# Kernel tuning notes

Hardware: AMD Instinct MI355X
Metric: run time of the kernel (lower is better)

Reference implementation:

```python
import jax, jax.numpy as jnp
import numpy as np

EMB = 1024
HEADS = 16


def setup_inputs() -> dict:
    key = jax.random.key(0)
    ks = jax.random.split(key, 9)
    s = 1.0 / np.sqrt(EMB)
    x = jax.random.normal(ks[0], (2, 2048, EMB), dtype=jnp.float32)
    Wq = jax.random.normal(ks[1], (EMB, EMB), dtype=jnp.float32) * s
    bq = jnp.zeros((EMB,), dtype=jnp.float32)
    Wk = jax.random.normal(ks[2], (EMB, EMB), dtype=jnp.float32) * s
    bk = jnp.zeros((EMB,), dtype=jnp.float32)
    Wv = jax.random.normal(ks[3], (EMB, EMB), dtype=jnp.float32) * s
    bv = jnp.zeros((EMB,), dtype=jnp.float32)
    Wo = jax.random.normal(ks[4], (EMB, EMB), dtype=jnp.float32) * s
    bo = jnp.zeros((EMB,), dtype=jnp.float32)
    return {"x": x, "Wq": Wq, "bq": bq, "Wk": Wk, "bk": bk,
            "Wv": Wv, "bv": bv, "Wo": Wo, "bo": bo}


def reference(x, Wq, bq, Wk, bk, Wv, bv, Wo, bo):
    b, n, e = x.shape
    h = HEADS
    d = e // h
    # q/k/v projections -> [b, h, n, d]
    def split_heads(t):
        return t.reshape(b, n, h, d).transpose(0, 2, 1, 3)
    q = split_heads(x @ Wq.T + bq)
    k = split_heads(x @ Wk.T + bk)
    v = split_heads(x @ Wv.T + bv)
    # NOTE: original scales by sqrt(emb_size), not sqrt(head_dim)
    scaling = jnp.sqrt(jnp.float32(e))
    energy = jnp.einsum('bhqd,bhkd->bhqk', q, k)  # [b,h,n,n]
    att = jax.nn.softmax(energy / scaling, axis=-1)
    out = jnp.einsum('bhqk,bhkd->bhqd', att, v)
    out = out.transpose(0, 2, 1, 3).reshape(b, n, e)
    return out @ Wo.T + bo
```

## Files before the change

### kernel.cpp

```cpp
#include <hip/hip_runtime.h>


typedef short short8  __attribute__((ext_vector_type(8)));
typedef float floatx4 __attribute__((ext_vector_type(4)));

#define SEQ   2048
#define BATCH 2
#define NH    16
#define HD    64
#define EMB   1024

#define QSCALE 0.045084220027780106f

__device__ __forceinline__ unsigned short f32_bf16(float f) {
    unsigned int u = __float_as_uint(f);
    u += 0x7FFF + ((u >> 16) & 1);
    return (unsigned short)(u >> 16);
}

__device__ __forceinline__ unsigned int pk_bf16(float lo, float hi) {
    return __builtin_amdgcn_perm(__float_as_uint(hi) + 0x8000u,
                                 __float_as_uint(lo) + 0x8000u, 0x07060302u);
}

__device__ __forceinline__ void gl_lds16(const unsigned short* g,
                                         unsigned short* l) {
    __builtin_amdgcn_global_load_lds(
        (const __attribute__((address_space(1))) unsigned int*)g,
        (__attribute__((address_space(3))) unsigned int*)l, 16, 0, 0);
}

__global__ __launch_bounds__(256) void convert_all(
        const float* __restrict__ x,  const float* __restrict__ wq,
        const float* __restrict__ wk, const float* __restrict__ wv,
        const float* __restrict__ wo, unsigned short* __restrict__ dst) {
    int i = (blockIdx.x * 256 + threadIdx.x) * 4;
    const float* src; int off;
    if      (i < 4194304) { src = x;  off = 0; }
    else if (i < 5242880) { src = wq; off = 4194304; }
    else if (i < 6291456) { src = wk; off = 5242880; }
    else if (i < 7340032) { src = wv; off = 6291456; }
    else                  { src = wo; off = 7340032; }
    float4 v = *(const float4*)(src + (i - off));
    uint2 o;
    o.x = pk_bf16(v.x, v.y);
    o.y = pk_bf16(v.z, v.w);
    *(uint2*)(dst + i) = o;
}

template <int MODE>
__device__ __forceinline__ void gemm_bt_core(
        unsigned short (* __restrict__ sA)[64],
        unsigned short (* __restrict__ sB)[64],
        const unsigned short* __restrict__ A,
        const unsigned short* __restrict__ B,
        const float* __restrict__ bias,
        unsigned short* __restrict__ outb) {
    const int t    = threadIdx.x;
    const int wave = t >> 6, lane = t & 63;
    const int l15  = lane & 15, quad = lane >> 4;
    const int wm   = (wave >> 1) * 64, wn = (wave & 1) * 64;
    const int m0   = blockIdx.y * 128,  n0 = blockIdx.x * 128;
    const int srow = lane >> 3;
    const int sch  = ((lane & 7) ^ srow) * 8;

    floatx4 acc[4][4] = {};

    for (int k0 = 0; k0 < EMB; k0 += 64) {
        for (int i = 0; i < 4; ++i) {
            int rr  = wave * 32 + i * 8;
            int row = rr + srow;
            gl_lds16(&A[(size_t)(m0 + row) * EMB + k0 + sch], &sA[0][0] + rr * 64);
            gl_lds16(&B[(size_t)(n0 + row) * EMB + k0 + sch], &sB[0][0] + rr * 64);
        }
        __syncthreads();
        for (int ks = 0; ks < 2; ++ks) {
            const int ch = (((ks * 4) + quad) ^ (l15 & 7)) * 8;
            short8 af[4], bf[4];
            for (int i = 0; i < 4; ++i)
                af[i] = *(const short8*)&sA[wm + i * 16 + l15][ch];
            for (int j = 0; j < 4; ++j)
                bf[j] = *(const short8*)&sB[wn + j * 16 + l15][ch];
            for (int i = 0; i < 4; ++i)
                for (int j = 0; j < 4; ++j)
                    acc[i][j] = __builtin_amdgcn_mfma_f32_16x16x32_bf16(
                        af[i], bf[j], acc[i][j], 0, 0, 0);
        }
        __syncthreads();
    }
    if (MODE == 2) {
        for (int i = 0; i < 4; ++i) {
            int row = m0 + wm + i * 16 + quad * 4;
            int bb  = row >> 11, seq = row & 2047;
            for (int j = 0; j < 4; ++j) {
                int col = n0 + wn + j * 16 + l15;
                float bv = bias[col];
                int vtrow = (bb * 16 + (col >> 6)) * 64 + (col & 63);
                uint2 pk;
                pk.x = pk_bf16(acc[i][j][0] + bv, acc[i][j][1] + bv);
                pk.y = pk_bf16(acc[i][j][2] + bv, acc[i][j][3] + bv);
                *(uint2*)&outb[(size_t)vtrow * SEQ + seq] = pk;
            }
        }
    } else {
        const float sc2 = (MODE == 1) ? QSCALE : 1.0f;
        for (int i = 0; i < 4; ++i) {
            int row = m0 + wm + i * 16 + quad * 4;
            for (int j = 0; j < 4; ++j) {
                int col = n0 + wn + j * 16 + l15;
                float bv = bias[col];
                for (int r = 0; r < 4; ++r) {
                    float v = (acc[i][j][r] + bv) * sc2;
                    outb[(size_t)(row + r) * EMB + col] = f32_bf16(v);
                }
            }
        }
    }
}

__global__ __launch_bounds__(256, 3) void gemm_qkv(
        const unsigned short* __restrict__ xb,
        const unsigned short* __restrict__ wq,
        const unsigned short* __restrict__ wk,
        const unsigned short* __restrict__ wv,
        const float* __restrict__ bq, const float* __restrict__ bk,
        const float* __restrict__ bv,
        unsigned short* __restrict__ Q, unsigned short* __restrict__ K,
        unsigned short* __restrict__ VT) {
    __shared__ unsigned short sA[128][64];
    __shared__ unsigned short sB[128][64];
    if      (blockIdx.z == 0) gemm_bt_core<1>(sA, sB, xb, wq, bq, Q);
    else if (blockIdx.z == 1) gemm_bt_core<0>(sA, sB, xb, wk, bk, K);
    else                      gemm_bt_core<2>(sA, sB, xb, wv, bv, VT);
}

__global__ __launch_bounds__(256) void gemm_out(
        const unsigned short* __restrict__ A,
        const unsigned short* __restrict__ B,
        const float* __restrict__ bias, float* __restrict__ out) {
    __shared__ unsigned short sA[128][64];
    __shared__ unsigned short sB[64][64];
    const int t    = threadIdx.x;
    const int wave = t >> 6, lane = t & 63;
    const int l15  = lane & 15, quad = lane >> 4;
    const int wm   = wave * 32;
    const int m0   = blockIdx.y * 128,  n0 = blockIdx.x * 64;
    const int srow = lane >> 3;
    const int sch  = ((lane & 7) ^ srow) * 8;

    floatx4 acc[2][4] = {};

    for (int k0 = 0; k0 < EMB; k0 += 64) {
        {
            for (int i = 0; i < 4; ++i) {
                int rr = wave * 32 + i * 8;
                gl_lds16(&A[(size_t)(m0 + rr + srow) * EMB + k0 + sch],
                         &sA[0][0] + rr * 64);
            }
            for (int i = 0; i < 2; ++i) {
                int rr = wave * 16 + i * 8;
                gl_lds16(&B[(size_t)(n0 + rr + srow) * EMB + k0 + sch],
                         &sB[0][0] + rr * 64);
            }
        }
        __syncthreads();
        for (int ks = 0; ks < 2; ++ks) {
            const int ch = (((ks * 4) + quad) ^ (l15 & 7)) * 8;
            short8 af[2], bf[4];
            for (int i = 0; i < 2; ++i)
                af[i] = *(const short8*)&sA[wm + i * 16 + l15][ch];
            for (int j = 0; j < 4; ++j)
                bf[j] = *(const short8*)&sB[j * 16 + l15][ch];
            for (int i = 0; i < 2; ++i)
                for (int j = 0; j < 4; ++j)
                    acc[i][j] = __builtin_amdgcn_mfma_f32_16x16x32_bf16(
                        af[i], bf[j], acc[i][j], 0, 0, 0);
        }
        __syncthreads();
    }
    for (int i = 0; i < 2; ++i) {
        int row = m0 + wm + i * 16 + quad * 4;
        for (int j = 0; j < 4; ++j) {
            int col = n0 + j * 16 + l15;
            float bv = bias[col];
            for (int r = 0; r < 4; ++r)
                out[(size_t)(row + r) * EMB + col] = acc[i][j][r] + bv;
        }
    }
}

__global__ __launch_bounds__(512) void attn(
        const unsigned short* __restrict__ Q,
        const unsigned short* __restrict__ K,
        const unsigned short* __restrict__ VT,
        unsigned short* __restrict__ O) {
    __shared__ unsigned short sK [3][64][64];
    __shared__ unsigned short sVT[3][64][64];
    __shared__ unsigned short sP [128][72];
    const int t    = threadIdx.x;
    const int wave = t >> 6, lane = t & 63;
    const int l15  = lane & 15, quad = lane >> 4;
    const int bh   = blockIdx.x;
    const int b    = bh >> 4, h = bh & 15;
    const int q0   = blockIdx.y * 128;
    const size_t rowbase = (size_t)b * SEQ;
    const int colbase  = h * HD;
    const size_t vtbase = (size_t)bh * HD * SEQ;
    const int srow = lane >> 3;
    const int sch  = ((lane & 7) ^ srow) * 8;

    short8 qf[2];
    for (int ks = 0; ks < 2; ++ks)
        qf[ks] = *(const short8*)&Q[(rowbase + q0 + wave * 16 + l15) * EMB
                                    + colbase + ks * 32 + quad * 8];

    float l_part = 0.f;
    floatx4 o_acc[4] = {};

    const int rr  = wave * 8;
    const int row = rr + srow;

    gl_lds16(&K[(rowbase + row) * EMB + colbase + sch], &sK[0][0][0] + rr * 64);
    gl_lds16(&VT[vtbase + (size_t)row * SEQ + sch],     &sVT[0][0][0] + rr * 64);

    int cur = 0;
    for (int it = 0; it < SEQ / 64; ++it) {
        if (it < SEQ / 64 - 1) {
            int nb = cur + 1; if (nb == 3) nb = 0;
            int kt = (it + 1) * 64;
            gl_lds16(&K[(rowbase + kt + row) * EMB + colbase + sch],
                     &sK[nb][0][0] + rr * 64);
            gl_lds16(&VT[vtbase + (size_t)row * SEQ + kt + sch],
                     &sVT[nb][0][0] + rr * 64);
            asm volatile("s_waitcnt vmcnt(2)" ::: "memory");
        } else {
            asm volatile("s_waitcnt vmcnt(0)" ::: "memory");
        }
        asm volatile("s_barrier" ::: "memory");

        const unsigned short (*cK)[64]  = sK[cur];
        const unsigned short (*cVT)[64] = sVT[cur];

        floatx4 s[4] = {};
        for (int ks = 0; ks < 2; ++ks) {
            const int ch = (((ks * 4) + quad) ^ (l15 & 7)) * 8;
            short8 kf[4];
            for (int mi = 0; mi < 4; ++mi)
                kf[mi] = *(const short8*)&cK[mi * 16 + l15][ch];
            for (int mi = 0; mi < 4; ++mi)
                s[mi] = __builtin_amdgcn_mfma_f32_16x16x32_bf16(
                    kf[mi], qf[ks], s[mi], 0, 0, 0);
        }

        {
            int prow = wave * 16 + l15;
            float lp = l_part;
            for (int mi = 0; mi < 4; ++mi) {
                float p0 = __builtin_amdgcn_exp2f(s[mi][0]);
                float p1 = __builtin_amdgcn_exp2f(s[mi][1]);
                float p2 = __builtin_amdgcn_exp2f(s[mi][2]);
                float p3 = __builtin_amdgcn_exp2f(s[mi][3]);
                lp += (p0 + p1) + (p2 + p3);
                uint2 pk;
                pk.x = pk_bf16(p0, p1);
                pk.y = pk_bf16(p2, p3);
                *(uint2*)&sP[prow][mi * 16 + quad * 4] = pk;
            }
            l_part = lp;
        }

        for (int ks = 0; ks < 2; ++ks) {
            const int ch = (((ks * 4) + quad) ^ (l15 & 7)) * 8;
            short8 vf[4];
            for (int mi = 0; mi < 4; ++mi)
                vf[mi] = *(const short8*)&cVT[mi * 16 + l15][ch];
            short8 pf = *(const short8*)&sP[wave * 16 + l15][ks * 32 + quad * 8];
            for (int mi = 0; mi < 4; ++mi)
                o_acc[mi] = __builtin_amdgcn_mfma_f32_16x16x32_bf16(
                    vf[mi], pf, o_acc[mi], 0, 0, 0);
        }
        cur = cur + 1; if (cur == 3) cur = 0;
    }

    float la = l_part;
    la += __shfl_xor(la, 16, 64);
    la += __shfl_xor(la, 32, 64);
    const float inv_l = 1.0f / la;

    {
        int prow = wave * 16 + l15;
        for (int mi = 0; mi < 4; ++mi) {
            uint2 pk;
            pk.x = pk_bf16(o_acc[mi][0] * inv_l, o_acc[mi][1] * inv_l);
            pk.y = pk_bf16(o_acc[mi][2] * inv_l, o_acc[mi][3] * inv_l);
            *(uint2*)&sP[prow][mi * 16 + quad * 4] = pk;
        }
    }
    __builtin_amdgcn_s_waitcnt(0);
    const int ql = lane >> 2, dh = (lane & 3) * 16;
    const size_t grow = rowbase + q0 + wave * 16 + ql;
    for (int i = 0; i < 2; ++i) {
        uint4 v = *(const uint4*)&sP[wave * 16 + ql][dh + i * 8];
        *(uint4*)&O[grow * EMB + colbase + dh + i * 8] = v;
    }
}

extern "C" void kernel_launch(void* const* d_in, const int* in_sizes, int n_in,
                              void* d_out, int out_size, void* d_ws, size_t ws_size,
                              hipStream_t stream) {
    const float* x  = (const float*)d_in[0];
    const float* Wq = (const float*)d_in[1];
    const float* bq = (const float*)d_in[2];
    const float* Wk = (const float*)d_in[3];
    const float* bk = (const float*)d_in[4];
    const float* Wv = (const float*)d_in[5];
    const float* bv = (const float*)d_in[6];
    const float* Wo = (const float*)d_in[7];
    const float* bo = (const float*)d_in[8];

    unsigned short* ws  = (unsigned short*)d_ws;
    unsigned short* xb  = ws;
    unsigned short* wqb = ws + 4194304;
    unsigned short* wkb = ws + 5242880;
    unsigned short* wvb = ws + 6291456;
    unsigned short* wob = ws + 7340032;
    unsigned short* Qb  = ws + 8388608;
    unsigned short* Kb  = ws + 12582912;
    unsigned short* VTb = ws + 16777216;
    unsigned short* Ob  = ws + 20971520;

    convert_all<<<8192, 256, 0, stream>>>(x, Wq, Wk, Wv, Wo, ws);
    gemm_qkv<<<dim3(8, 32, 3), 256, 0, stream>>>(xb, wqb, wkb, wvb,
                                                 bq, bk, bv, Qb, Kb, VTb);
    attn<<<dim3(32, 16), 512, 0, stream>>>(Qb, Kb, VTb, Ob);
    gemm_out<<<dim3(16, 32), 256, 0, stream>>>(Ob, wob, bo, (float*)d_out);
}
```

Measured before the change: 184.2 us.

## Give each attention wave two 16-row query groups with 256-thread blocks

The attention kernel now runs 4 waves per block instead of 8, and each wave handles 32 query rows as two 16-row groups. Each K and V^T fragment read from LDS feeds twice as many MFMAs, and each wave issues two async K/V tile loads per buffer instead of one. This cuts LDS read traffic and barrier participants per unit of work. In exchange it doubles per-wave accumulator and score registers and halves the number of waves per block, which may reduce latency hiding.

```diff
diff --git a/kernel.cpp b/kernel.cpp
--- a/kernel.cpp
+++ b/kernel.cpp
@@ -189,7 +189,7 @@
     }
 }
 
-__global__ __launch_bounds__(512) void attn(
+__global__ __launch_bounds__(256) void attn(
         const unsigned short* __restrict__ Q,
         const unsigned short* __restrict__ K,
         const unsigned short* __restrict__ VT,
@@ -209,30 +209,39 @@
     const int srow = lane >> 3;
     const int sch  = ((lane & 7) ^ srow) * 8;
 
-    short8 qf[2];
-    for (int ks = 0; ks < 2; ++ks)
-        qf[ks] = *(const short8*)&Q[(rowbase + q0 + wave * 16 + l15) * EMB
-                                    + colbase + ks * 32 + quad * 8];
-
-    float l_part = 0.f;
-    floatx4 o_acc[4] = {};
-
-    const int rr  = wave * 8;
-    const int row = rr + srow;
-
-    gl_lds16(&K[(rowbase + row) * EMB + colbase + sch], &sK[0][0][0] + rr * 64);
-    gl_lds16(&VT[vtbase + (size_t)row * SEQ + sch],     &sVT[0][0][0] + rr * 64);
+    short8 qf[2][2];
+    for (int g = 0; g < 2; ++g)
+        for (int ks = 0; ks < 2; ++ks)
+            qf[g][ks] = *(const short8*)
+                &Q[(rowbase + q0 + wave * 32 + g * 16 + l15) * EMB
+                   + colbase + ks * 32 + quad * 8];
+
+    float l_part[2] = {0.f, 0.f};
+    floatx4 o_acc[2][4] = {};
+
+    for (int i = 0; i < 2; ++i) {
+        int rr  = wave * 16 + i * 8;
+        int row = rr + srow;
+        gl_lds16(&K[(rowbase + row) * EMB + colbase + sch],
+                 &sK[0][0][0] + rr * 64);
+        gl_lds16(&VT[vtbase + (size_t)row * SEQ + sch],
+                 &sVT[0][0][0] + rr * 64);
+    }
 
     int cur = 0;
     for (int it = 0; it < SEQ / 64; ++it) {
         if (it < SEQ / 64 - 1) {
             int nb = cur + 1; if (nb == 3) nb = 0;
             int kt = (it + 1) * 64;
-            gl_lds16(&K[(rowbase + kt + row) * EMB + colbase + sch],
-                     &sK[nb][0][0] + rr * 64);
-            gl_lds16(&VT[vtbase + (size_t)row * SEQ + kt + sch],
-                     &sVT[nb][0][0] + rr * 64);
-            asm volatile("s_waitcnt vmcnt(2)" ::: "memory");
+            for (int i = 0; i < 2; ++i) {
+                int rr  = wave * 16 + i * 8;
+                int row = rr + srow;
+                gl_lds16(&K[(rowbase + kt + row) * EMB + colbase + sch],
+                         &sK[nb][0][0] + rr * 64);
+                gl_lds16(&VT[vtbase + (size_t)row * SEQ + kt + sch],
+                         &sVT[nb][0][0] + rr * 64);
+            }
+            asm volatile("s_waitcnt vmcnt(4)" ::: "memory");
         } else {
             asm volatile("s_waitcnt vmcnt(0)" ::: "memory");
         }
@@ -241,32 +250,33 @@
         const unsigned short (*cK)[64]  = sK[cur];
         const unsigned short (*cVT)[64] = sVT[cur];
 
-        floatx4 s[4] = {};
+        floatx4 s[2][4] = {};
         for (int ks = 0; ks < 2; ++ks) {
             const int ch = (((ks * 4) + quad) ^ (l15 & 7)) * 8;
             short8 kf[4];
             for (int mi = 0; mi < 4; ++mi)
                 kf[mi] = *(const short8*)&cK[mi * 16 + l15][ch];
-            for (int mi = 0; mi < 4; ++mi)
-                s[mi] = __builtin_amdgcn_mfma_f32_16x16x32_bf16(
-                    kf[mi], qf[ks], s[mi], 0, 0, 0);
-        }
-
-        {
-            int prow = wave * 16 + l15;
-            float lp = l_part;
+            for (int g = 0; g < 2; ++g)
+                for (int mi = 0; mi < 4; ++mi)
+                    s[g][mi] = __builtin_amdgcn_mfma_f32_16x16x32_bf16(
+                        kf[mi], qf[g][ks], s[g][mi], 0, 0, 0);
+        }
+
+        for (int g = 0; g < 2; ++g) {
+            int prow = wave * 32 + g * 16 + l15;
+            float lp = l_part[g];
             for (int mi = 0; mi < 4; ++mi) {
-                float p0 = __builtin_amdgcn_exp2f(s[mi][0]);
-                float p1 = __builtin_amdgcn_exp2f(s[mi][1]);
-                float p2 = __builtin_amdgcn_exp2f(s[mi][2]);
-                float p3 = __builtin_amdgcn_exp2f(s[mi][3]);
+                float p0 = __builtin_amdgcn_exp2f(s[g][mi][0]);
+                float p1 = __builtin_amdgcn_exp2f(s[g][mi][1]);
+                float p2 = __builtin_amdgcn_exp2f(s[g][mi][2]);
+                float p3 = __builtin_amdgcn_exp2f(s[g][mi][3]);
                 lp += (p0 + p1) + (p2 + p3);
                 uint2 pk;
                 pk.x = pk_bf16(p0, p1);
                 pk.y = pk_bf16(p2, p3);
                 *(uint2*)&sP[prow][mi * 16 + quad * 4] = pk;
             }
-            l_part = lp;
+            l_part[g] = lp;
         }
 
         for (int ks = 0; ks < 2; ++ks) {
@@ -274,34 +284,38 @@
             short8 vf[4];
             for (int mi = 0; mi < 4; ++mi)
                 vf[mi] = *(const short8*)&cVT[mi * 16 + l15][ch];
-            short8 pf = *(const short8*)&sP[wave * 16 + l15][ks * 32 + quad * 8];
-            for (int mi = 0; mi < 4; ++mi)
-                o_acc[mi] = __builtin_amdgcn_mfma_f32_16x16x32_bf16(
-                    vf[mi], pf, o_acc[mi], 0, 0, 0);
+            for (int g = 0; g < 2; ++g) {
+                short8 pf = *(const short8*)
+                    &sP[wave * 32 + g * 16 + l15][ks * 32 + quad * 8];
+                for (int mi = 0; mi < 4; ++mi)
+                    o_acc[g][mi] = __builtin_amdgcn_mfma_f32_16x16x32_bf16(
+                        vf[mi], pf, o_acc[g][mi], 0, 0, 0);
+            }
         }
         cur = cur + 1; if (cur == 3) cur = 0;
     }
 
-    float la = l_part;
-    la += __shfl_xor(la, 16, 64);
-    la += __shfl_xor(la, 32, 64);
-    const float inv_l = 1.0f / la;
-
-    {
-        int prow = wave * 16 + l15;
+    for (int g = 0; g < 2; ++g) {
+        float la = l_part[g];
+        la += __shfl_xor(la, 16, 64);
+        la += __shfl_xor(la, 32, 64);
+        const float inv_l = 1.0f / la;
+        int prow = wave * 32 + g * 16 + l15;
         for (int mi = 0; mi < 4; ++mi) {
             uint2 pk;
-            pk.x = pk_bf16(o_acc[mi][0] * inv_l, o_acc[mi][1] * inv_l);
-            pk.y = pk_bf16(o_acc[mi][2] * inv_l, o_acc[mi][3] * inv_l);
+            pk.x = pk_bf16(o_acc[g][mi][0] * inv_l, o_acc[g][mi][1] * inv_l);
+            pk.y = pk_bf16(o_acc[g][mi][2] * inv_l, o_acc[g][mi][3] * inv_l);
             *(uint2*)&sP[prow][mi * 16 + quad * 4] = pk;
         }
     }
     __builtin_amdgcn_s_waitcnt(0);
     const int ql = lane >> 2, dh = (lane & 3) * 16;
-    const size_t grow = rowbase + q0 + wave * 16 + ql;
-    for (int i = 0; i < 2; ++i) {
-        uint4 v = *(const uint4*)&sP[wave * 16 + ql][dh + i * 8];
-        *(uint4*)&O[grow * EMB + colbase + dh + i * 8] = v;
+    for (int g = 0; g < 2; ++g) {
+        const size_t grow = rowbase + q0 + wave * 32 + g * 16 + ql;
+        for (int i = 0; i < 2; ++i) {
+            uint4 v = *(const uint4*)&sP[wave * 32 + g * 16 + ql][dh + i * 8];
+            *(uint4*)&O[grow * EMB + colbase + dh + i * 8] = v;
+        }
     }
 }
 
@@ -332,6 +346,6 @@
     convert_all<<<8192, 256, 0, stream>>>(x, Wq, Wk, Wv, Wo, ws);
     gemm_qkv<<<dim3(8, 32, 3), 256, 0, stream>>>(xb, wqb, wkb, wvb,
                                                  bq, bk, bv, Qb, Kb, VTb);
-    attn<<<dim3(32, 16), 512, 0, stream>>>(Qb, Kb, VTb, Ob);
+    attn<<<dim3(32, 16), 256, 0, stream>>>(Qb, Kb, VTb, Ob);
     gemm_out<<<dim3(16, 32), 256, 0, stream>>>(Ob, wob, bo, (float*)d_out);
 }
```

Measured after the change: 191.0 us. 3.7% more time.
